# Kernel tuning notes

Hardware: AMD Instinct MI355X
Metric: run time of the kernel (lower is better)

Reference implementation:

```python
import jax, jax.numpy as jnp
import numpy as np

B, C, H, W = 16, 256, 64, 64
K = 1024


def setup_inputs() -> dict:
    key = jax.random.key(0)
    k1, k2 = jax.random.split(key)
    z = jax.random.normal(k1, (B, C, H, W), dtype=jnp.float32)
    codebook = jax.random.normal(k2, (K, C), dtype=jnp.float32)
    return {"z": z, "codebook": codebook}


def reference(z, codebook):
    # assign: nearest-code indices via squared euclidean distance
    b, c, h, w = z.shape
    zf = jnp.transpose(z, (0, 2, 3, 1)).reshape(-1, c)            # [N, C]
    # ||z||^2 - 2 z.cb^T + ||cb||^2  -> [N, K]
    dists = (jnp.sum(zf * zf, axis=1, keepdims=True)
             - 2.0 * jnp.einsum('nc,kc->nk', zf, codebook)
             + jnp.sum(codebook * codebook, axis=1)[None, :])
    idx = jnp.argmin(dists, axis=1)                                # [N]
    indices = idx.reshape(b, 1, h, w)                              # [B,1,H,W]
    # embed_code: gather codebook rows, back to BCHW
    zq = codebook[idx].reshape(b, h, w, c)                         # [B,H,W,C]
    zq = jnp.transpose(zq, (0, 3, 1, 2))                           # [B,C,H,W]
    return zq, indices
```

## Files before the change

kernel.cpp:

```cpp
#include <hip/hip_runtime.h>


#define HWSZ 4096
#define CDIM 256
#define KCODES 1024
#define NPIX 65536
#define ZQ_ELEMS (16 * 256 * 4096)
#define MARGIN 0.75f

#define WS_CBSWZ 0
#define WS_CBN64 524288
#define WS_CBN32 532480
#define WS_CNT   536576
#define WS_LISTS 536592

#define L_BUF0   0
#define L_NRM    49152
#define L_MK     53248
#define L_SBEST  56320
#define L_FLP    56832
#define L_FLQ    57344
#define L_LCNT   57856
#define L_TOTAL  58368

typedef __attribute__((ext_vector_type(8))) short bf16x8;
typedef __attribute__((ext_vector_type(4))) float f32x4;
typedef __attribute__((ext_vector_type(4))) unsigned short us4;

#define MFMA16(a, b, c) __builtin_amdgcn_mfma_f32_16x16x32_bf16(a, b, c, 0, 0, 0)

__device__ __forceinline__ unsigned short f2bf(float f) {
  unsigned u = __float_as_uint(f);
  unsigned r = u + 0x7FFFu + ((u >> 16) & 1u);
  return (unsigned short)(r >> 16);
}

__device__ __forceinline__ unsigned cvtpk(float lo, float hi) {
  unsigned r;
  asm("v_cvt_pk_bf16_f32 %0, %1, %2" : "=v"(r) : "v"(lo), "v"(hi));
  return r;
}

__device__ __forceinline__ void gload_lds16(const void* g, void* l) {
  __builtin_amdgcn_global_load_lds(
      (const __attribute__((address_space(1))) unsigned int*)g,
      (__attribute__((address_space(3))) unsigned int*)l, 16, 0, 0);
}

__device__ __forceinline__ void ins3(unsigned& k1, unsigned& k2, unsigned& k3,
                                     unsigned k) {
  unsigned nk2, nk3;
  asm("v_med3_u32 %0, %1, %2, %3" : "=v"(nk2) : "v"(k1), "v"(k2), "v"(k));
  asm("v_med3_u32 %0, %1, %2, %3" : "=v"(nk3) : "v"(k2), "v"(k3), "v"(k));
  k1 = k1 < k ? k1 : k;
  k2 = nk2;
  k3 = nk3;
}

__device__ __forceinline__ float keyf(unsigned k) {
  return __uint_as_float(k & 0xFFFFFC00u);
}

__global__ void vq_prep(const float* __restrict__ cb,
                        unsigned short* __restrict__ cbswz,
                        double* __restrict__ cbn64,
                        float* __restrict__ cbn32p,
                        int* __restrict__ cnt) {
  const int t = threadIdx.x;
  if (blockIdx.x == 0 && t == 0) { cnt[0] = 0; cnt[1] = 0; }
  const int code = blockIdx.x * 4 + (t >> 6);
  const int lane = t & 63;
  const int c4 = lane * 4;

  float4 v = *(const float4*)(cb + (size_t)code * CDIM + c4);
  us4 hv;
  hv.x = f2bf(-2.f * v.x); hv.y = f2bf(-2.f * v.y);
  hv.z = f2bf(-2.f * v.z); hv.w = f2bf(-2.f * v.w);
  const int K = (code >> 9) * 32 + ((code >> 4) & 31);
  const int kk = c4 >> 5;
  const int lg = (c4 >> 3) & 3;
  const int within = (c4 & 7) * 2;
  size_t off = (size_t)K * 8192 + kk * 1024 + (code & 15) * 64 + lg * 16 + within;
  *(us4*)((char*)cbswz + off) = hv;

  double s = (double)v.x * v.x;
  s = fma((double)v.y, (double)v.y, s);
  s = fma((double)v.z, (double)v.z, s);
  s = fma((double)v.w, (double)v.w, s);
#pragma unroll
  for (int o = 32; o; o >>= 1) s += __shfl_xor(s, o, 64);
  if (lane == 0) {
    cbn64[code] = s;
    cbn32p[code] = (float)s + 512.0f;
  }
}

__launch_bounds__(256, 2)
__global__ void vq_stage1(const float* __restrict__ z,
                          const float* __restrict__ cb,
                          const unsigned short* __restrict__ cbswz,
                          const float* __restrict__ cbn32p,
                          float* __restrict__ out_zq,
                          float* __restrict__ out_idx,
                          int* __restrict__ cnt,
                          int* __restrict__ listA, int capA,
                          int* __restrict__ listB, int capB,
                          float* __restrict__ zws, int zcap) {
  extern __shared__ char smem[];
  const int t = threadIdx.x;
  const int w = t >> 6;
  const int lane = t & 63;
  const int lg = lane >> 4;
  const int lcode = lane & 15;
  const int h = w >> 1;
  const int q = w & 1;
  const int p0 = blockIdx.x * 128;
  const int b = p0 >> 12;
  const int hw0 = p0 & (HWSZ - 1);
  const float* zb = z + (size_t)b * (CDIM * HWSZ) + hw0;

  char* const bb0 = smem + q * 8192;
  char* const bb1 = smem + 16384 + q * 8192;
  char* const bb2 = smem + 32768 + q * 8192;
  float* nrm = (float*)(smem + L_NRM);

  const int stl = h * 4096 + lane * 16;
  const char* cbbase = (const char*)cbswz + (size_t)q * 262144 + stl;

#define STAGE(CIDX, SBUF)                                             \
  {                                                                   \
    const char* gs_ = cbbase + ((size_t)(CIDX) << 13);                \
    char* ld_ = (SBUF) + stl;                                         \
    gload_lds16(gs_, ld_);                                            \
    gload_lds16(gs_ + 1024, ld_ + 1024);                              \
    gload_lds16(gs_ + 2048, ld_ + 2048);                              \
    gload_lds16(gs_ + 3072, ld_ + 3072);                              \
  }

  STAGE(0, bb0);
  STAGE(1, bb1);

  bf16x8 af[4][8];
#pragma unroll
  for (int T = 0; T < 4; ++T) {
    const float* zr = zb + (h * 64 + T * 16 + lcode);
#pragma unroll
    for (int kk = 0; kk < 8; ++kk) {
      const int ch0 = kk * 32 + lg * 8;
      float v0 = zr[(size_t)(ch0 + 0) * HWSZ];
      float v1 = zr[(size_t)(ch0 + 1) * HWSZ];
      float v2 = zr[(size_t)(ch0 + 2) * HWSZ];
      float v3 = zr[(size_t)(ch0 + 3) * HWSZ];
      float v4 = zr[(size_t)(ch0 + 4) * HWSZ];
      float v5 = zr[(size_t)(ch0 + 5) * HWSZ];
      float v6 = zr[(size_t)(ch0 + 6) * HWSZ];
      float v7 = zr[(size_t)(ch0 + 7) * HWSZ];
      unsigned p01 = cvtpk(v0, v1);
      unsigned p23 = cvtpk(v2, v3);
      unsigned p45 = cvtpk(v4, v5);
      unsigned p67 = cvtpk(v6, v7);
      bf16x8 f;
      f[0] = (short)(p01 & 0xFFFF); f[1] = (short)(p01 >> 16);
      f[2] = (short)(p23 & 0xFFFF); f[3] = (short)(p23 >> 16);
      f[4] = (short)(p45 & 0xFFFF); f[5] = (short)(p45 >> 16);
      f[6] = (short)(p67 & 0xFFFF); f[7] = (short)(p67 >> 16);
      af[T][kk] = f;
    }
  }

  *(float4*)(nrm + t * 4) = *(const float4*)(cbn32p + t * 4);
  __syncthreads();

  unsigned k1[4][4], k2[4][4], k3[4][4];
#pragma unroll
  for (int T = 0; T < 4; ++T)
#pragma unroll
    for (int q4 = 0; q4 < 4; ++q4) {
      k1[T][q4] = 0xFFFFFFFFu; k2[T][q4] = 0xFFFFFFFFu; k3[T][q4] = 0xFFFFFFFFu;
    }

  const int bq = lcode * 64 + lg * 16;
  const float* nrmp = nrm + q * 512 + lcode;
  const int kbase = q * 512 + lcode;
  float cnn = nrmp[0];

#define BODY(CIDX, RBUF, SBUF, DOSTAGE, WN)                           \
  {                                                                   \
    asm volatile("s_waitcnt vmcnt(" WN ")" ::: "memory");             \
    __builtin_amdgcn_s_barrier();                                     \
    __builtin_amdgcn_sched_barrier(0);                                \
    const float cn_ = cnn;                                            \
    if ((CIDX) < 31) cnn = nrmp[((CIDX) + 1) * 16];                   \
    if (DOSTAGE) STAGE((CIDX) + 2, SBUF);                             \
    const char* pb_ = (RBUF) + bq;                                    \
    f32x4 a0 = {cn_, cn_, cn_, cn_};                                  \
    f32x4 a1 = {cn_, cn_, cn_, cn_};                                  \
    f32x4 a2 = {cn_, cn_, cn_, cn_};                                  \
    f32x4 a3 = {cn_, cn_, cn_, cn_};                                  \
    _Pragma("unroll")                                                 \
    for (int kk = 0; kk < 8; ++kk) {                                  \
      bf16x8 bf_ = *(const bf16x8*)(pb_ + kk * 1024);                 \
      a0 = MFMA16(af[0][kk], bf_, a0);                                \
      a1 = MFMA16(af[1][kk], bf_, a1);                                \
      a2 = MFMA16(af[2][kk], bf_, a2);                                \
      a3 = MFMA16(af[3][kk], bf_, a3);                                \
    }                                                                 \
    const unsigned code_ = (unsigned)(kbase + (CIDX) * 16);           \
    _Pragma("unroll")                                                 \
    for (int q4 = 0; q4 < 4; ++q4) {                                  \
      ins3(k1[0][q4], k2[0][q4], k3[0][q4],                           \
           (__float_as_uint(a0[q4]) & 0xFFFFFC00u) | code_);          \
      ins3(k1[1][q4], k2[1][q4], k3[1][q4],                           \
           (__float_as_uint(a1[q4]) & 0xFFFFFC00u) | code_);          \
      ins3(k1[2][q4], k2[2][q4], k3[2][q4],                           \
           (__float_as_uint(a2[q4]) & 0xFFFFFC00u) | code_);          \
      ins3(k1[3][q4], k2[3][q4], k3[3][q4],                           \
           (__float_as_uint(a3[q4]) & 0xFFFFFC00u) | code_);          \
    }                                                                 \
  }

#pragma unroll 1
  for (int c3 = 0; c3 < 30; c3 += 3) {
    BODY(c3 + 0, bb0, bb2, 1, "4");
    BODY(c3 + 1, bb1, bb0, 1, "4");
    BODY(c3 + 2, bb2, bb1, 1, "4");
  }
  BODY(30, bb0, bb2, 0, "4");
  BODY(31, bb1, bb0, 0, "0");
#undef BODY
#undef STAGE

#pragma unroll
  for (int mask = 1; mask <= 8; mask <<= 1) {
#pragma unroll
    for (int T = 0; T < 4; ++T)
#pragma unroll
      for (int q4 = 0; q4 < 4; ++q4) {
        unsigned o1 = __shfl_xor(k1[T][q4], mask, 64);
        unsigned o2 = __shfl_xor(k2[T][q4], mask, 64);
        unsigned o3 = __shfl_xor(k3[T][q4], mask, 64);
        ins3(k1[T][q4], k2[T][q4], k3[T][q4], o1);
        ins3(k1[T][q4], k2[T][q4], k3[T][q4], o2);
        ins3(k1[T][q4], k2[T][q4], k3[T][q4], o3);
      }
  }

  unsigned* mk = (unsigned*)(smem + L_MK);
  int* sbest = (int*)(smem + L_SBEST);
  int* flp = (int*)(smem + L_FLP);
  int* flq = (int*)(smem + L_FLQ);
  int* lcnt = (int*)(smem + L_LCNT);
  if (t == 0) *lcnt = 0;
  if (lcode == 0) {
#pragma unroll
    for (int T = 0; T < 4; ++T)
#pragma unroll
      for (int q4 = 0; q4 < 4; ++q4) {
        int row = h * 64 + T * 16 + lg * 4 + q4;
        unsigned* d = mk + (row * 2 + q) * 3;
        d[0] = k1[T][q4]; d[1] = k2[T][q4]; d[2] = k3[T][q4];
      }
  }
  __syncthreads();

  if (t < 128) {
    unsigned a1 = mk[t * 6 + 0], a2 = mk[t * 6 + 1], a3 = mk[t * 6 + 2];
    ins3(a1, a2, a3, mk[t * 6 + 3]);
    ins3(a1, a2, a3, mk[t * 6 + 4]);
    ins3(a1, a2, a3, mk[t * 6 + 5]);
    const int p = p0 + t;
    const int i1 = (int)(a1 & 1023u);
    sbest[t] = i1;
    out_idx[p] = (float)i1;
    float f1 = keyf(a1);
    float g2 = keyf(a2) - f1;
    float g3 = keyf(a3) - f1;
    if (g3 < MARGIN) {
      int pos = atomicAdd(cnt + 1, 1);
      if (pos < capB) listB[pos] = p;
    } else if (g2 < MARGIN) {
      int pos = atomicAdd(cnt, 1);
      if (pos < capA) {
        listA[2 * pos] = p | (i1 << 16);
        listA[2 * pos + 1] = (int)(a2 & 1023u) | ((int)(a3 & 1023u) << 16);
        if (pos < zcap) {
          int li = atomicAdd(lcnt, 1);
          flp[li] = p;
          flq[li] = pos;
        }
      }
    }
  }
  __syncthreads();

  {
    const int px = t & 127;
    const int best = sbest[px];
    const int ch0g = (t >> 7) * 128;
    const float* crow = cb + (size_t)best * CDIM + ch0g;
    float* ob = out_zq + (size_t)b * (CDIM * HWSZ) + (size_t)ch0g * HWSZ + hw0 + px;
#pragma unroll 4
    for (int c2 = 0; c2 < 128; c2 += 4) {
      float4 v = *(const float4*)(crow + c2);
      ob[(size_t)(c2 + 0) * HWSZ] = v.x;
      ob[(size_t)(c2 + 1) * HWSZ] = v.y;
      ob[(size_t)(c2 + 2) * HWSZ] = v.z;
      ob[(size_t)(c2 + 3) * HWSZ] = v.w;
    }
  }

  {
    const int nf = *lcnt;
    for (int e = 0; e < nf; ++e) {
      const int p = flp[e];
      const int slot = flq[e];
      const int bb = p >> 12;
      const int hh = p & (HWSZ - 1);
      zws[(size_t)slot * 256 + t] =
          z[(size_t)bb * (CDIM * HWSZ) + (size_t)t * HWSZ + hh];
    }
  }
}

__launch_bounds__(256)
__global__ void vq_resolve3(const float* __restrict__ z,
                            const float* __restrict__ cb,
                            const double* __restrict__ cbn64,
                            float* __restrict__ out_zq,
                            float* __restrict__ out_idx,
                            const int* __restrict__ cnt,
                            const int* __restrict__ listA, int capA,
                            const float* __restrict__ zws, int zcap) {
  const int lane = threadIdx.x & 63;
  const int wid = (blockIdx.x * blockDim.x + threadIdx.x) >> 6;
  const int nw = (gridDim.x * blockDim.x) >> 6;
  int n = cnt[0];
  if (n > capA) n = capA;

  for (int i = wid; i < n; i += nw) {
    const int e0 = listA[2 * i];
    const int e1 = listA[2 * i + 1];
    const int p = e0 & 0xFFFF;
    int cand[3];
    cand[0] = (e0 >> 16) & 1023;
    cand[1] = e1 & 0xFFFF;
    cand[2] = (e1 >> 16) & 1023;
    const int b = p >> 12;
    const int hw = p & (HWSZ - 1);
    const int ch0 = lane * 4;

    double zv[4];
    if (i < zcap) {
      float4 zf = ((const float4*)(zws + (size_t)i * 256))[lane];
      zv[0] = (double)zf.x; zv[1] = (double)zf.y;
      zv[2] = (double)zf.z; zv[3] = (double)zf.w;
    } else {
      const float* zb = z + (size_t)b * (CDIM * HWSZ) + hw;
#pragma unroll
      for (int j = 0; j < 4; ++j) zv[j] = (double)zb[(size_t)(ch0 + j) * HWSZ];
    }

    double d[3];
#pragma unroll
    for (int tt = 0; tt < 3; ++tt) {
      float4 cv = *(const float4*)(cb + (size_t)cand[tt] * CDIM + ch0);
      double s = zv[0] * (double)cv.x;
      s = fma(zv[1], (double)cv.y, s);
      s = fma(zv[2], (double)cv.z, s);
      s = fma(zv[3], (double)cv.w, s);
#pragma unroll
      for (int off = 32; off; off >>= 1) s += __shfl_xor(s, off, 64);
      d[tt] = fma(-2.0, s, cbn64[cand[tt]]);
    }

    double bd = d[0];
    int bi = cand[0];
#pragma unroll
    for (int tt = 1; tt < 3; ++tt) {
      bool takes = (d[tt] < bd) || (d[tt] == bd && cand[tt] < bi);
      bd = takes ? d[tt] : bd;
      bi = takes ? cand[tt] : bi;
    }

    if (bi != cand[0]) {
      if (lane == 0) out_idx[p] = (float)bi;
      float4 cv = *(const float4*)(cb + (size_t)bi * CDIM + ch0);
      float* ob = out_zq + (size_t)b * (CDIM * HWSZ) + hw;
      ob[(size_t)(ch0 + 0) * HWSZ] = cv.x;
      ob[(size_t)(ch0 + 1) * HWSZ] = cv.y;
      ob[(size_t)(ch0 + 2) * HWSZ] = cv.z;
      ob[(size_t)(ch0 + 3) * HWSZ] = cv.w;
    }
  }
}

__launch_bounds__(256)
__global__ void vq_fullscan(const float* __restrict__ z,
                            const float* __restrict__ cb,
                            const double* __restrict__ cbn64,
                            float* __restrict__ out_zq,
                            float* __restrict__ out_idx,
                            const int* __restrict__ cnt,
                            const int* __restrict__ listB, int capB) {
  __shared__ double zl[256];
  __shared__ double sd[4];
  __shared__ int si[4];
  __shared__ int sfin;
  int n = cnt[1];
  if (n > capB) n = capB;
  const int t = threadIdx.x;
  const int w = t >> 6;
  const int lane = t & 63;

  for (int i = blockIdx.x; i < n; i += gridDim.x) {
    const int p = listB[i];
    const int b = p >> 12;
    const int hw = p & (HWSZ - 1);
    const float* zb = z + (size_t)b * (CDIM * HWSZ) + hw;
    zl[t] = (double)zb[(size_t)t * HWSZ];
    __syncthreads();

    const int g = t >> 2;
    const int sub = t & 3;
    const double* zq4 = zl + sub * 64;
    double bd = 1e300;
    int bi = 0;

    for (int j = 0; j < 16; ++j) {
      const int code = g + 64 * j;
      const float* crow = cb + (size_t)code * CDIM + sub * 64;
      double s = 0.0;
#pragma unroll
      for (int q4 = 0; q4 < 64; q4 += 4) {
        float4 cv = *(const float4*)(crow + q4);
        s = fma(zq4[q4 + 0], (double)cv.x, s);
        s = fma(zq4[q4 + 1], (double)cv.y, s);
        s = fma(zq4[q4 + 2], (double)cv.z, s);
        s = fma(zq4[q4 + 3], (double)cv.w, s);
      }
      s += __shfl_xor(s, 1, 64);
      s += __shfl_xor(s, 2, 64);
      double d = fma(-2.0, s, cbn64[code]);
      bool takes = (d < bd) || (d == bd && code < bi);
      bd = takes ? d : bd;
      bi = takes ? code : bi;
    }

#pragma unroll
    for (int off = 4; off <= 32; off <<= 1) {
      double od = __shfl_xor(bd, off, 64);
      int oi = __shfl_xor(bi, off, 64);
      bool takes = (od < bd) || (od == bd && oi < bi);
      bd = takes ? od : bd;
      bi = takes ? oi : bi;
    }
    if (lane == 0) { sd[w] = bd; si[w] = bi; }
    __syncthreads();
    if (t == 0) {
      double fd = sd[0];
      int fi = si[0];
#pragma unroll
      for (int k = 1; k < 4; ++k) {
        bool takes = (sd[k] < fd) || (sd[k] == fd && si[k] < fi);
        fd = takes ? sd[k] : fd;
        fi = takes ? si[k] : fi;
      }
      const int old = (int)out_idx[p];
      sfin = (fi != old) ? fi : -1;
      if (fi != old) out_idx[p] = (float)fi;
    }
    __syncthreads();
    const int best = sfin;
    if (best >= 0) {
      float* ob = out_zq + (size_t)b * (CDIM * HWSZ) + hw;
      ob[(size_t)t * HWSZ] = cb[(size_t)best * CDIM + t];
    }
    __syncthreads();
  }
}

extern "C" void kernel_launch(void* const* d_in, const int* in_sizes, int n_in,
                              void* d_out, int out_size, void* d_ws, size_t ws_size,
                              hipStream_t stream) {
  const float* z = (const float*)d_in[0];
  const float* cb = (const float*)d_in[1];
  float* out = (float*)d_out;
  float* out_zq = out;
  float* out_idx = out + ZQ_ELEMS;

  char* ws = (char*)d_ws;
  unsigned short* cbswz = (unsigned short*)(ws + WS_CBSWZ);
  double* cbn64 = (double*)(ws + WS_CBN64);
  float* cbn32p = (float*)(ws + WS_CBN32);
  int* cnt = (int*)(ws + WS_CNT);

  long long avail = (long long)ws_size - WS_LISTS;
  if (avail < 0) avail = 0;
  long long capA_ll = (avail / 4) / 8;
  if (capA_ll > NPIX) capA_ll = NPIX;
  int capA = (int)capA_ll;
  int* listA = (int*)(ws + WS_LISTS);
  long long rem = avail - (long long)capA * 8;
  long long capB_ll = rem / 8;
  if (capB_ll > NPIX) capB_ll = NPIX;
  if (capB_ll < 0) capB_ll = 0;
  int capB = (int)capB_ll;
  int* listB = (int*)(ws + WS_LISTS + (size_t)capA * 8);
  long long zoff = (WS_LISTS + (long long)capA * 8 + (long long)capB * 4 + 15) &
                   ~15LL;
  long long zcap_ll = ((long long)ws_size - zoff) / 1024;
  if (zcap_ll < 0) zcap_ll = 0;
  if (zcap_ll > capA) zcap_ll = capA;
  int zcap = (int)zcap_ll;
  float* zws = (float*)(ws + zoff);

  vq_prep<<<256, 256, 0, stream>>>(cb, cbswz, cbn64, cbn32p, cnt);
  vq_stage1<<<512, 256, L_TOTAL, stream>>>(z, cb, cbswz, cbn32p, out_zq, out_idx,
                                           cnt, listA, capA, listB, capB,
                                           zws, zcap);
  vq_resolve3<<<1024, 256, 0, stream>>>(z, cb, cbn64, out_zq, out_idx,
                                        cnt, listA, capA, zws, zcap);
  vq_fullscan<<<256, 256, 0, stream>>>(z, cb, cbn64, out_zq, out_idx,
                                       cnt, listB, capB);
}
```

Baseline: 150.6 us.

## Deepen codebook LDS pipeline to four buffers and merge fix-up kernels

Stage 1 now triple-prefetches codebook tiles into a fourth LDS buffer: the prefetch distance grows from 2 to 3 and the waitcnt thresholds change to match. The MFMA section is wrapped in s_setprio, and the dynamic LDS size is raised to about 73KB through hipFuncSetAttribute. The two follow-up kernels (three-candidate resolve and full rescan) are merged into one launch with 256 blocks, removing a kernel launch. More LDS per block may cut occupancy, and the resolve pass now runs on fewer waves (1024 instead of 4096).

```diff
diff --git a/kernel.cpp b/kernel.cpp
--- a/kernel.cpp
+++ b/kernel.cpp
@@ -14,14 +14,13 @@
 #define WS_CNT   536576
 #define WS_LISTS 536592
 
-#define L_BUF0   0
-#define L_NRM    49152
-#define L_MK     53248
-#define L_SBEST  56320
-#define L_FLP    56832
-#define L_FLQ    57344
-#define L_LCNT   57856
-#define L_TOTAL  58368
+#define L_NRM    65536
+#define L_MK     69632
+#define L_SBEST  72704
+#define L_FLP    73216
+#define L_FLQ    73728
+#define L_LCNT   74240
+#define L_TOTAL  74496
 
 typedef __attribute__((ext_vector_type(8))) short bf16x8;
 typedef __attribute__((ext_vector_type(4))) float f32x4;
@@ -122,6 +121,7 @@
   char* const bb0 = smem + q * 8192;
   char* const bb1 = smem + 16384 + q * 8192;
   char* const bb2 = smem + 32768 + q * 8192;
+  char* const bb3 = smem + 49152 + q * 8192;
   float* nrm = (float*)(smem + L_NRM);
 
   const int stl = h * 4096 + lane * 16;
@@ -139,6 +139,7 @@
 
   STAGE(0, bb0);
   STAGE(1, bb1);
+  STAGE(2, bb2);
 
   bf16x8 af[4][8];
 #pragma unroll
@@ -191,12 +192,13 @@
     __builtin_amdgcn_sched_barrier(0);                                \
     const float cn_ = cnn;                                            \
     if ((CIDX) < 31) cnn = nrmp[((CIDX) + 1) * 16];                   \
-    if (DOSTAGE) STAGE((CIDX) + 2, SBUF);                             \
+    if (DOSTAGE) STAGE((CIDX) + 3, SBUF);                             \
     const char* pb_ = (RBUF) + bq;                                    \
     f32x4 a0 = {cn_, cn_, cn_, cn_};                                  \
     f32x4 a1 = {cn_, cn_, cn_, cn_};                                  \
     f32x4 a2 = {cn_, cn_, cn_, cn_};                                  \
     f32x4 a3 = {cn_, cn_, cn_, cn_};                                  \
+    __builtin_amdgcn_s_setprio(1);                                    \
     _Pragma("unroll")                                                 \
     for (int kk = 0; kk < 8; ++kk) {                                  \
       bf16x8 bf_ = *(const bf16x8*)(pb_ + kk * 1024);                 \
@@ -205,6 +207,7 @@
       a2 = MFMA16(af[2][kk], bf_, a2);                                \
       a3 = MFMA16(af[3][kk], bf_, a3);                                \
     }                                                                 \
+    __builtin_amdgcn_s_setprio(0);                                    \
     const unsigned code_ = (unsigned)(kbase + (CIDX) * 16);           \
     _Pragma("unroll")                                                 \
     for (int q4 = 0; q4 < 4; ++q4) {                                  \
@@ -220,13 +223,16 @@
   }
 
 #pragma unroll 1
-  for (int c3 = 0; c3 < 30; c3 += 3) {
-    BODY(c3 + 0, bb0, bb2, 1, "4");
-    BODY(c3 + 1, bb1, bb0, 1, "4");
-    BODY(c3 + 2, bb2, bb1, 1, "4");
-  }
-  BODY(30, bb0, bb2, 0, "4");
-  BODY(31, bb1, bb0, 0, "0");
+  for (int c4 = 0; c4 < 28; c4 += 4) {
+    BODY(c4 + 0, bb0, bb3, 1, "8");
+    BODY(c4 + 1, bb1, bb0, 1, "8");
+    BODY(c4 + 2, bb2, bb1, 1, "8");
+    BODY(c4 + 3, bb3, bb2, 1, "8");
+  }
+  BODY(28, bb0, bb3, 1, "8");
+  BODY(29, bb1, bb0, 0, "8");
+  BODY(30, bb2, bb1, 0, "4");
+  BODY(31, bb3, bb2, 0, "0");
 #undef BODY
 #undef STAGE
 
@@ -323,94 +329,88 @@
 }
 
 __launch_bounds__(256)
-__global__ void vq_resolve3(const float* __restrict__ z,
-                            const float* __restrict__ cb,
-                            const double* __restrict__ cbn64,
-                            float* __restrict__ out_zq,
-                            float* __restrict__ out_idx,
-                            const int* __restrict__ cnt,
-                            const int* __restrict__ listA, int capA,
-                            const float* __restrict__ zws, int zcap) {
-  const int lane = threadIdx.x & 63;
-  const int wid = (blockIdx.x * blockDim.x + threadIdx.x) >> 6;
-  const int nw = (gridDim.x * blockDim.x) >> 6;
-  int n = cnt[0];
-  if (n > capA) n = capA;
-
-  for (int i = wid; i < n; i += nw) {
-    const int e0 = listA[2 * i];
-    const int e1 = listA[2 * i + 1];
-    const int p = e0 & 0xFFFF;
-    int cand[3];
-    cand[0] = (e0 >> 16) & 1023;
-    cand[1] = e1 & 0xFFFF;
-    cand[2] = (e1 >> 16) & 1023;
-    const int b = p >> 12;
-    const int hw = p & (HWSZ - 1);
-    const int ch0 = lane * 4;
-
-    double zv[4];
-    if (i < zcap) {
-      float4 zf = ((const float4*)(zws + (size_t)i * 256))[lane];
-      zv[0] = (double)zf.x; zv[1] = (double)zf.y;
-      zv[2] = (double)zf.z; zv[3] = (double)zf.w;
-    } else {
-      const float* zb = z + (size_t)b * (CDIM * HWSZ) + hw;
-#pragma unroll
-      for (int j = 0; j < 4; ++j) zv[j] = (double)zb[(size_t)(ch0 + j) * HWSZ];
-    }
-
-    double d[3];
-#pragma unroll
-    for (int tt = 0; tt < 3; ++tt) {
-      float4 cv = *(const float4*)(cb + (size_t)cand[tt] * CDIM + ch0);
-      double s = zv[0] * (double)cv.x;
-      s = fma(zv[1], (double)cv.y, s);
-      s = fma(zv[2], (double)cv.z, s);
-      s = fma(zv[3], (double)cv.w, s);
-#pragma unroll
-      for (int off = 32; off; off >>= 1) s += __shfl_xor(s, off, 64);
-      d[tt] = fma(-2.0, s, cbn64[cand[tt]]);
-    }
-
-    double bd = d[0];
-    int bi = cand[0];
-#pragma unroll
-    for (int tt = 1; tt < 3; ++tt) {
-      bool takes = (d[tt] < bd) || (d[tt] == bd && cand[tt] < bi);
-      bd = takes ? d[tt] : bd;
-      bi = takes ? cand[tt] : bi;
-    }
-
-    if (bi != cand[0]) {
-      if (lane == 0) out_idx[p] = (float)bi;
-      float4 cv = *(const float4*)(cb + (size_t)bi * CDIM + ch0);
-      float* ob = out_zq + (size_t)b * (CDIM * HWSZ) + hw;
-      ob[(size_t)(ch0 + 0) * HWSZ] = cv.x;
-      ob[(size_t)(ch0 + 1) * HWSZ] = cv.y;
-      ob[(size_t)(ch0 + 2) * HWSZ] = cv.z;
-      ob[(size_t)(ch0 + 3) * HWSZ] = cv.w;
-    }
-  }
-}
-
-__launch_bounds__(256)
-__global__ void vq_fullscan(const float* __restrict__ z,
-                            const float* __restrict__ cb,
-                            const double* __restrict__ cbn64,
-                            float* __restrict__ out_zq,
-                            float* __restrict__ out_idx,
-                            const int* __restrict__ cnt,
-                            const int* __restrict__ listB, int capB) {
+__global__ void vq_fix(const float* __restrict__ z,
+                       const float* __restrict__ cb,
+                       const double* __restrict__ cbn64,
+                       float* __restrict__ out_zq,
+                       float* __restrict__ out_idx,
+                       const int* __restrict__ cnt,
+                       const int* __restrict__ listA, int capA,
+                       const float* __restrict__ zws, int zcap,
+                       const int* __restrict__ listB, int capB) {
+  const int t = threadIdx.x;
+  const int w = t >> 6;
+  const int lane = t & 63;
+
+  {
+    const int wid = blockIdx.x * 4 + w;
+    const int nw = gridDim.x * 4;
+    int n = cnt[0];
+    if (n > capA) n = capA;
+
+    for (int i = wid; i < n; i += nw) {
+      const int e0 = listA[2 * i];
+      const int e1 = listA[2 * i + 1];
+      const int p = e0 & 0xFFFF;
+      int cand[3];
+      cand[0] = (e0 >> 16) & 1023;
+      cand[1] = e1 & 0xFFFF;
+      cand[2] = (e1 >> 16) & 1023;
+      const int b = p >> 12;
+      const int hw = p & (HWSZ - 1);
+      const int ch0 = lane * 4;
+
+      double zv[4];
+      if (i < zcap) {
+        float4 zf = ((const float4*)(zws + (size_t)i * 256))[lane];
+        zv[0] = (double)zf.x; zv[1] = (double)zf.y;
+        zv[2] = (double)zf.z; zv[3] = (double)zf.w;
+      } else {
+        const float* zb = z + (size_t)b * (CDIM * HWSZ) + hw;
+#pragma unroll
+        for (int j = 0; j < 4; ++j) zv[j] = (double)zb[(size_t)(ch0 + j) * HWSZ];
+      }
+
+      double d[3];
+#pragma unroll
+      for (int tt = 0; tt < 3; ++tt) {
+        float4 cv = *(const float4*)(cb + (size_t)cand[tt] * CDIM + ch0);
+        double s = zv[0] * (double)cv.x;
+        s = fma(zv[1], (double)cv.y, s);
+        s = fma(zv[2], (double)cv.z, s);
+        s = fma(zv[3], (double)cv.w, s);
+#pragma unroll
+        for (int off = 32; off; off >>= 1) s += __shfl_xor(s, off, 64);
+        d[tt] = fma(-2.0, s, cbn64[cand[tt]]);
+      }
+
+      double bd = d[0];
+      int bi = cand[0];
+#pragma unroll
+      for (int tt = 1; tt < 3; ++tt) {
+        bool takes = (d[tt] < bd) || (d[tt] == bd && cand[tt] < bi);
+        bd = takes ? d[tt] : bd;
+        bi = takes ? cand[tt] : bi;
+      }
+
+      if (bi != cand[0]) {
+        if (lane == 0) out_idx[p] = (float)bi;
+        float4 cv = *(const float4*)(cb + (size_t)bi * CDIM + ch0);
+        float* ob = out_zq + (size_t)b * (CDIM * HWSZ) + hw;
+        ob[(size_t)(ch0 + 0) * HWSZ] = cv.x;
+        ob[(size_t)(ch0 + 1) * HWSZ] = cv.y;
+        ob[(size_t)(ch0 + 2) * HWSZ] = cv.z;
+        ob[(size_t)(ch0 + 3) * HWSZ] = cv.w;
+      }
+    }
+  }
+
   __shared__ double zl[256];
   __shared__ double sd[4];
   __shared__ int si[4];
   __shared__ int sfin;
   int n = cnt[1];
   if (n > capB) n = capB;
-  const int t = threadIdx.x;
-  const int w = t >> 6;
-  const int lane = t & 63;
 
   for (int i = blockIdx.x; i < n; i += gridDim.x) {
     const int p = listB[i];
@@ -514,12 +514,13 @@
   int zcap = (int)zcap_ll;
   float* zws = (float*)(ws + zoff);
 
+  hipFuncSetAttribute(reinterpret_cast<const void*>(vq_stage1),
+                      hipFuncAttributeMaxDynamicSharedMemorySize, L_TOTAL);
+
   vq_prep<<<256, 256, 0, stream>>>(cb, cbswz, cbn64, cbn32p, cnt);
   vq_stage1<<<512, 256, L_TOTAL, stream>>>(z, cb, cbswz, cbn32p, out_zq, out_idx,
                                            cnt, listA, capA, listB, capB,
                                            zws, zcap);
-  vq_resolve3<<<1024, 256, 0, stream>>>(z, cb, cbn64, out_zq, out_idx,
-                                        cnt, listA, capA, zws, zcap);
-  vq_fullscan<<<256, 256, 0, stream>>>(z, cb, cbn64, out_zq, out_idx,
-                                       cnt, listB, capB);
-}
+  vq_fix<<<256, 256, 0, stream>>>(z, cb, cbn64, out_zq, out_idx,
+                                  cnt, listA, capA, zws, zcap, listB, capB);
+}
```

Result: slower. 155.0 us (+2.9%).
